# Optimization experiments

Measured on AMD Instinct MI355X. Metric: run time of the kernel, lower is better.

Reference implementation:

```python
import jax, jax.numpy as jnp
import numpy as np

N = 12288      # 12 * nside^2, nside=32
NBR = 20       # HEALpix graph neighbors
E = N * (NBR + 1)
B = 4
CIN = 8
COUT = 8
EPS = 1e-5


def _spmm(vals, row, col, x):
    """y = L @ x per batch/channel. x: [B, V, C]; L sparse COO (row, col, vals)."""
    b, v, c = x.shape
    x2 = x.transpose(1, 0, 2).reshape(v, b * c)          # [V, B*C]
    y = jax.ops.segment_sum(x2[col] * vals[:, None], row, num_segments=v)
    return y.reshape(v, b, c).transpose(1, 0, 2)          # [B, V, C]


def _cheb(vals, row, col, x, w, bias):
    """Chebyshev spectral graph conv: sum_k T_k(L) x W_k + b. w: [K, Fin, Fout]."""
    K = w.shape[0]
    xs = [x]
    if K > 1:
        xs.append(_spmm(vals, row, col, x))
    for _ in range(2, K):
        xs.append(2.0 * _spmm(vals, row, col, xs[-1]) - xs[-2])
    xk = jnp.stack(xs)                                    # [K, B, V, Fin]
    return jnp.einsum('kbvi,kio->bvo', xk, w) + bias


def _bn(x, g, b):
    # BatchNorm1d in training mode: stats over (batch, vertex) per channel
    m = x.mean(axis=(0, 1))
    v = x.var(axis=(0, 1))
    return (x - m) * jax.lax.rsqrt(v + EPS) * g + b


def setup_inputs() -> dict:
    key = jax.random.key(0)
    ks = jax.random.split(key, 12)
    x = jax.random.normal(ks[0], (B, N, CIN), jnp.float32)
    row = jnp.repeat(jnp.arange(N, dtype=jnp.int32), NBR + 1)
    nbr = jax.random.randint(ks[1], (N, NBR), 0, N, dtype=jnp.int32)
    col = jnp.concatenate([jnp.arange(N, dtype=jnp.int32)[:, None], nbr], axis=1).reshape(-1)
    edge_val = jax.random.normal(ks[2], (E,), jnp.float32) * 0.1

    def w(k, shape):
        return jax.random.normal(k, shape, jnp.float32) * 0.05

    return dict(
        x=x, edge_row=row, edge_col=col, edge_val=edge_val,
        conv1_w=w(ks[3], (3, CIN, 64)), conv1_b=jnp.zeros((64,), jnp.float32),
        bn1_g=jnp.ones((64,), jnp.float32), bn1_b=jnp.zeros((64,), jnp.float32),
        conv2_w=w(ks[4], (3, 64, 256)), conv2_b=jnp.zeros((256,), jnp.float32),
        bn2_g=jnp.ones((256,), jnp.float32), bn2_b=jnp.zeros((256,), jnp.float32),
        # 3 identical-shape bottlenecks stacked on leading axis
        bt_c1w=w(ks[5], (3, 1, 256, 64)), bt_c1b=jnp.zeros((3, 64), jnp.float32),
        bt_c2w=w(ks[6], (3, 3, 64, 64)), bt_c2b=jnp.zeros((3, 64), jnp.float32),
        bt_c3w=w(ks[7], (3, 1, 64, 256)), bt_c3b=jnp.zeros((3, 256), jnp.float32),
        bt_bn1g=jnp.ones((3, 64), jnp.float32), bt_bn1b=jnp.zeros((3, 64), jnp.float32),
        bt_bn2g=jnp.ones((3, 64), jnp.float32), bt_bn2b=jnp.zeros((3, 64), jnp.float32),
        bt_bn3g=jnp.ones((3, 256), jnp.float32), bt_bn3b=jnp.zeros((3, 256), jnp.float32),
        conv3_w=w(ks[8], (3, 256, COUT)), conv3_b=jnp.zeros((COUT,), jnp.float32),
    )


def reference(x, edge_row, edge_col, edge_val,
              conv1_w, conv1_b, bn1_g, bn1_b,
              conv2_w, conv2_b, bn2_g, bn2_b,
              bt_c1w, bt_c1b, bt_c2w, bt_c2b, bt_c3w, bt_c3b,
              bt_bn1g, bt_bn1b, bt_bn2g, bt_bn2b, bt_bn3g, bt_bn3b,
              conv3_w, conv3_b):
    L = (edge_val, edge_row, edge_col)

    def conv_block(h, w_, b_, g, bb):
        h = _cheb(*L, h, w_, b_)
        return jax.nn.relu(_bn(h, g, bb))

    def bottleneck(h, i):
        y = _cheb(*L, h, bt_c1w[i], bt_c1b[i])
        y = jax.nn.relu(_bn(y, bt_bn1g[i], bt_bn1b[i]))
        y = _cheb(*L, y, bt_c2w[i], bt_c2b[i])
        y = jax.nn.relu(_bn(y, bt_bn2g[i], bt_bn2b[i]))
        y = _cheb(*L, y, bt_c3w[i], bt_c3b[i])
        return _bn(y, bt_bn3g[i], bt_bn3b[i])

    h = conv_block(x, conv1_w, conv1_b, bn1_g, bn1_b)
    h = conv_block(h, conv2_w, conv2_b, bn2_g, bn2_b)
    for i in range(3):  # fixed, structurally distinct bottleneck blocks
        h = h + bottleneck(h, i)
    return _cheb(*L, h, conv3_w, conv3_b)  # [B, N, COUT]
```

## Files before the change

### kernel.cpp

```cpp
#include <hip/hip_runtime.h>

static constexpr int NBRS = 21;
static constexpr int Nv   = 12288;
static constexpr int BV   = 4 * Nv;
static constexpr int NE   = Nv * NBRS;
static constexpr float BN_EPS = 1e-5f;

typedef __bf16 bf16x4 __attribute__((ext_vector_type(4)));
typedef __bf16 bf16x8 __attribute__((ext_vector_type(8)));
typedef float  f32x4  __attribute__((ext_vector_type(4)));

__device__ __forceinline__ int xcd_swz(int bid, int grid)
{
    return (bid & 7) * (grid >> 3) + (bid >> 3);
}

template<int MODE>
__global__ __launch_bounds__(256)
void spmm8_kernel(float* __restrict__ y, const float* __restrict__ x,
                  const float* __restrict__ x0,
                  const int2* __restrict__ edges)
{
    int idx = xcd_swz(blockIdx.x, gridDim.x) * 256 + threadIdx.x;
    int c4 = idx & 1;
    int row = idx >> 1;
    int v = row % Nv;
    int b = row / Nv;
    int e0 = v * NBRS;
    const float4* x4 = (const float4*)x;
    float4 acc = {0.f, 0.f, 0.f, 0.f};
    #pragma unroll
    for (int j = 0; j < NBRS; ++j) {
        const int2 ed = edges[e0 + j];
        const float a = __int_as_float(ed.x);
        const int u = ed.y;
        float4 xv = x4[(size_t)(b * Nv + u) * 2 + c4];
        acc.x = fmaf(a, xv.x, acc.x);
        acc.y = fmaf(a, xv.y, acc.y);
        acc.z = fmaf(a, xv.z, acc.z);
        acc.w = fmaf(a, xv.w, acc.w);
    }
    if (MODE == 2) {
        float4 p = ((const float4*)x0)[idx];
        acc.x += p.x; acc.y += p.y; acc.z += p.z; acc.w += p.w;
    }
    ((float4*)y)[idx] = acc;
}

template<bool BNG>
__global__ __launch_bounds__(256)
void spmm64_kernel(__bf16* __restrict__ y, const __bf16* __restrict__ x,
                   const int2* __restrict__ edges,
                   const float* __restrict__ bn_a, const float* __restrict__ bn_b)
{
    int idx = xcd_swz(blockIdx.x, gridDim.x) * 256 + threadIdx.x;
    int q = idx % 8;
    int v = (idx / 8) % Nv;
    int b = idx / (8 * Nv);
    int e0 = v * NBRS;
    const bf16x8* x8 = (const bf16x8*)x;
    float4 aL, aH, bL, bH;
    if (BNG) {
        aL = ((const float4*)bn_a)[q * 2];     aH = ((const float4*)bn_a)[q * 2 + 1];
        bL = ((const float4*)bn_b)[q * 2];     bH = ((const float4*)bn_b)[q * 2 + 1];
    }
    float acc[8];
    #pragma unroll
    for (int t = 0; t < 8; ++t) acc[t] = 0.f;
    #pragma unroll
    for (int j = 0; j < NBRS; ++j) {
        const int2 ed = edges[e0 + j];
        const float a = __int_as_float(ed.x);
        const int u = ed.y;
        bf16x8 hv = x8[(size_t)(b * Nv + u) * 8 + q];
        float xv[8];
        #pragma unroll
        for (int t = 0; t < 8; ++t) xv[t] = (float)hv[t];
        if (BNG) {
            xv[0] = fmaxf(fmaf(xv[0], aL.x, bL.x), 0.f);
            xv[1] = fmaxf(fmaf(xv[1], aL.y, bL.y), 0.f);
            xv[2] = fmaxf(fmaf(xv[2], aL.z, bL.z), 0.f);
            xv[3] = fmaxf(fmaf(xv[3], aL.w, bL.w), 0.f);
            xv[4] = fmaxf(fmaf(xv[4], aH.x, bH.x), 0.f);
            xv[5] = fmaxf(fmaf(xv[5], aH.y, bH.y), 0.f);
            xv[6] = fmaxf(fmaf(xv[6], aH.z, bH.z), 0.f);
            xv[7] = fmaxf(fmaf(xv[7], aH.w, bH.w), 0.f);
        }
        #pragma unroll
        for (int t = 0; t < 8; ++t) acc[t] = fmaf(a, xv[t], acc[t]);
    }
    bf16x8 o;
    #pragma unroll
    for (int t = 0; t < 8; ++t) o[t] = (__bf16)acc[t];
    ((bf16x8*)y)[idx] = o;
}

__global__ __launch_bounds__(256)
void pack_all_kernel(const float* __restrict__ w1, const float* __restrict__ w2,
                     const float* __restrict__ c1, const float* __restrict__ c2,
                     const float* __restrict__ c3, const float* __restrict__ w3,
                     const float* __restrict__ b3,
                     const float* __restrict__ eval_, const int* __restrict__ col,
                     __bf16* __restrict__ wb, float* __restrict__ bpack,
                     int2* __restrict__ edges)
{
    int t = blockIdx.x * 256 + threadIdx.x;
    if (t >= 194560) {
        int i = t - 194560;
        if (i < 32) { bpack[i] = (i < 8) ? b3[i] : 0.f; return; }
        int e = t - 194592;
        if (e < NE) edges[e] = make_int2(__float_as_int(eval_[e]), col[e]);
        return;
    }
    const float* src; int KSRC, FOUT, FIN, local; bool fold = false, isW3 = false;
    if (t < 2048)        { src = w1;  KSRC = 24;  FOUT = 64;  FIN = 8;  local = t; fold = true; }
    else if (t < 51200)  { src = w2;  KSRC = 192; FOUT = 256; FIN = 64; local = t - 2048; fold = true; }
    else if (t < 100352) { int i = (t - 51200) / 16384;  src = c1 + (size_t)i * 16384;
                           KSRC = 256; FOUT = 64;  FIN = 256; local = (t - 51200) % 16384; }
    else if (t < 137216) { int i = (t - 100352) / 12288; src = c2 + (size_t)i * 12288;
                           KSRC = 192; FOUT = 64;  FIN = 64; local = (t - 100352) % 12288; fold = true; }
    else if (t < 186368) { int i = (t - 137216) / 16384; src = c3 + (size_t)i * 16384;
                           KSRC = 64;  FOUT = 256; FIN = 64; local = (t - 137216) % 16384; }
    else                 { src = w3;  KSRC = 256; FOUT = 32; FIN = 256; local = t - 186368; isW3 = true; }
    const int j    = local & 7;
    const int lane = (local >> 3) & 63;
    const int rest = local >> 9;
    const int NT = FOUT >> 4;
    const int nt = rest % NT;
    const int ks = rest / NT;
    const int k = ks * 32 + (lane >> 4) * 8 + j;
    const int o = nt * 16 + (lane & 15);
    float v = 0.f;
    if (isW3) {
        const int zj = o >> 3, oo = o & 7;
        if (zj == 0)      v = src[(size_t)k * 8 + oo] - src[(size_t)2 * 2048 + k * 8 + oo];
        else if (zj == 1) v = src[(size_t)2048 + k * 8 + oo];
        else if (zj == 2) v = 2.f * src[(size_t)2 * 2048 + k * 8 + oo];
    } else if (k < KSRC) {
        if (fold) {
            if (k < FIN)          v = src[(size_t)k * FOUT + o] - src[(size_t)(k + 2 * FIN) * FOUT + o];
            else if (k < 2 * FIN) v = src[(size_t)k * FOUT + o];
            else                  v = 2.f * src[(size_t)k * FOUT + o];
        } else {
            v = src[(size_t)k * FOUT + o];
        }
    }
    wb[t] = (__bf16)v;
}

template<int FOUT, int KFIN, int KPAD, int FIN, int NSRC,
         bool STATS, bool BN0, bool HAS_BIAS, bool PACKOUT, bool INBF, bool OUTBF,
         bool RESID = false, bool BASEBN = false, bool WRITEBACK = false>
__global__ __launch_bounds__(256)
void gemm_mfma_kernel(const void* __restrict__ x0, const void* __restrict__ x1,
                      const void* __restrict__ x2,
                      const __bf16* __restrict__ wp, const float* __restrict__ bias,
                      const float* __restrict__ bn_a, const float* __restrict__ bn_b,
                      const float* __restrict__ bn_a2, const float* __restrict__ bn_b2,
                      void* __restrict__ out, float2* __restrict__ partial,
                      __bf16* __restrict__ wbk)
{
    constexpr int NT    = FOUT / 16;
    constexpr int NSTEP = KPAD / 32;
    constexpr bool COLS = (NT % 4 == 0);
    constexpr int NT2   = COLS ? NT / 4 : NT;
    constexpr int LDKB  = KPAD + 8;
    constexpr int LDC   = FOUT + 4;
    constexpr size_t XS_B  = (size_t)64 * LDKB * 2;
    constexpr size_t RPK_B = COLS ? (size_t)16 * LDC * 4 : 0;
    constexpr size_t SMEM  = XS_B > RPK_B ? XS_B : RPK_B;
    __shared__ __align__(16) char smem[SMEM];
    __bf16* xs = (__bf16*)smem;

    const int tid = threadIdx.x;
    const int m0 = blockIdx.x * 64;

    constexpr int NF4 = 64 * (KPAD / 4);
    for (int f = tid; f < NF4; f += 256) {
        const int r  = f / (KPAD / 4);
        const int ki = (f % (KPAD / 4)) * 4;
        bf16x4 h;
        if (KFIN == KPAD || ki < KFIN) {
            int i; int kk;
            if constexpr (NSRC == 1) { i = ki; kk = 0; }
            else { kk = ki / FIN; i = ki % FIN; }
            if constexpr (RESID) {
                const __bf16* srcy = (const __bf16*)x0;
                const __bf16* srct = (const __bf16*)x1;
                bf16x4 hy = *(const bf16x4*)(srcy + (size_t)(m0 + r) * FIN + i);
                bf16x4 ht = *(const bf16x4*)(srct + (size_t)(m0 + r) * FIN + i);
                const float4 a4 = *(const float4*)(bn_a + i);
                const float4 b4 = *(const float4*)(bn_b + i);
                float bv0 = (float)ht[0], bv1 = (float)ht[1];
                float bv2 = (float)ht[2], bv3 = (float)ht[3];
                if constexpr (BASEBN) {
                    const float4 p4 = *(const float4*)(bn_a2 + i);
                    const float4 q4 = *(const float4*)(bn_b2 + i);
                    bv0 = fmaxf(fmaf(bv0, p4.x, q4.x), 0.f);
                    bv1 = fmaxf(fmaf(bv1, p4.y, q4.y), 0.f);
                    bv2 = fmaxf(fmaf(bv2, p4.z, q4.z), 0.f);
                    bv3 = fmaxf(fmaf(bv3, p4.w, q4.w), 0.f);
                }
                h[0] = (__bf16)(fmaf((float)hy[0], a4.x, b4.x) + bv0);
                h[1] = (__bf16)(fmaf((float)hy[1], a4.y, b4.y) + bv1);
                h[2] = (__bf16)(fmaf((float)hy[2], a4.z, b4.z) + bv2);
                h[3] = (__bf16)(fmaf((float)hy[3], a4.w, b4.w) + bv3);
                if constexpr (WRITEBACK)
                    *(bf16x4*)(wbk + (size_t)(m0 + r) * FIN + i) = h;
            } else if constexpr (INBF) {
                const __bf16* src = (kk == 0) ? (const __bf16*)x0
                                  : (kk == 1 ? (const __bf16*)x1 : (const __bf16*)x2);
                bf16x4 hv = *(const bf16x4*)(src + (size_t)(m0 + r) * FIN + i);
                if (BN0 && (NSRC == 1 || kk == 0)) {
                    const float4 a4 = *(const float4*)(bn_a + i);
                    const float4 b4 = *(const float4*)(bn_b + i);
                    h[0] = (__bf16)fmaxf(fmaf((float)hv[0], a4.x, b4.x), 0.f);
                    h[1] = (__bf16)fmaxf(fmaf((float)hv[1], a4.y, b4.y), 0.f);
                    h[2] = (__bf16)fmaxf(fmaf((float)hv[2], a4.z, b4.z), 0.f);
                    h[3] = (__bf16)fmaxf(fmaf((float)hv[3], a4.w, b4.w), 0.f);
                } else {
                    h = hv;
                }
            } else {
                const float* src = (kk == 0) ? (const float*)x0
                                 : (kk == 1 ? (const float*)x1 : (const float*)x2);
                float4 v = *(const float4*)(src + (size_t)(m0 + r) * FIN + i);
                if (BN0 && (NSRC == 1 || kk == 0)) {
                    const float4 a4 = *(const float4*)(bn_a + i);
                    const float4 b4 = *(const float4*)(bn_b + i);
                    v.x = fmaxf(fmaf(v.x, a4.x, b4.x), 0.f);
                    v.y = fmaxf(fmaf(v.y, a4.y, b4.y), 0.f);
                    v.z = fmaxf(fmaf(v.z, a4.z, b4.z), 0.f);
                    v.w = fmaxf(fmaf(v.w, a4.w, b4.w), 0.f);
                }
                h[0] = (__bf16)v.x; h[1] = (__bf16)v.y; h[2] = (__bf16)v.z; h[3] = (__bf16)v.w;
            }
        } else {
            h[0] = (__bf16)0.f; h[1] = (__bf16)0.f; h[2] = (__bf16)0.f; h[3] = (__bf16)0.f;
        }
        *(bf16x4*)(xs + (size_t)r * LDKB + ki) = h;
    }
    __syncthreads();

    const int lane = tid & 63;
    const int wv   = tid >> 6;
    const int lo   = lane & 15;
    const int hi   = lane >> 4;

    if constexpr (COLS) {
        f32x4 acc[4][NT2];
        #pragma unroll
        for (int mr = 0; mr < 4; ++mr)
            #pragma unroll
            for (int n = 0; n < NT2; ++n) acc[mr][n] = (f32x4){0.f, 0.f, 0.f, 0.f};

        #pragma unroll
        for (int ks = 0; ks < NSTEP; ++ks) {
            bf16x8 bfr[NT2];
            #pragma unroll
            for (int n = 0; n < NT2; ++n)
                bfr[n] = *(const bf16x8*)(wp + ((size_t)(ks * NT + wv * NT2 + n) * 64 + lane) * 8);
            bf16x8 afr[4];
            #pragma unroll
            for (int mr = 0; mr < 4; ++mr)
                afr[mr] = *(const bf16x8*)(xs + (size_t)(mr * 16 + lo) * LDKB + ks * 32 + hi * 8);
            #pragma unroll
            for (int n = 0; n < NT2; ++n)
                #pragma unroll
                for (int mr = 0; mr < 4; ++mr)
                    acc[mr][n] = __builtin_amdgcn_mfma_f32_16x16x32_bf16(afr[mr], bfr[n], acc[mr][n], 0, 0, 0);
        }

        #pragma unroll
        for (int n = 0; n < NT2; ++n) {
            const int o = wv * (FOUT / 4) + n * 16 + lo;
            const float bo = HAS_BIAS ? bias[o] : 0.f;
            #pragma unroll
            for (int mr = 0; mr < 4; ++mr)
                #pragma unroll
                for (int j = 0; j < 4; ++j) acc[mr][n][j] += bo;
        }

        if constexpr (STATS) {
            #pragma unroll
            for (int n = 0; n < NT2; ++n) {
                float s = 0.f, q = 0.f;
                #pragma unroll
                for (int mr = 0; mr < 4; ++mr)
                    #pragma unroll
                    for (int j = 0; j < 4; ++j) {
                        const float v = acc[mr][n][j];
                        s += v; q = fmaf(v, v, q);
                    }
                s += __shfl_xor(s, 16); q += __shfl_xor(q, 16);
                s += __shfl_xor(s, 32); q += __shfl_xor(q, 32);
                if (lane < 16) {
                    const int o = wv * (FOUT / 4) + n * 16 + lo;
                    partial[(size_t)o * gridDim.x + blockIdx.x] = make_float2(s, q);
                }
            }
        }

        float* cs = (float*)smem;
        #pragma unroll
        for (int mr = 0; mr < 4; ++mr) {
            __syncthreads();
            #pragma unroll
            for (int n = 0; n < NT2; ++n) {
                const int o = wv * (FOUT / 4) + n * 16 + lo;
                #pragma unroll
                for (int j = 0; j < 4; ++j)
                    cs[(size_t)(hi * 4 + j) * LDC + o] = acc[mr][n][j];
            }
            __syncthreads();
            for (int t = tid; t < 16 * (FOUT / 4); t += 256) {
                const int rr = t / (FOUT / 4);
                const int c4 = (t % (FOUT / 4)) * 4;
                const float4 v = *(const float4*)(cs + (size_t)rr * LDC + c4);
                if constexpr (OUTBF) {
                    bf16x4 hv;
                    hv[0] = (__bf16)v.x; hv[1] = (__bf16)v.y;
                    hv[2] = (__bf16)v.z; hv[3] = (__bf16)v.w;
                    *(bf16x4*)((__bf16*)out + (size_t)(m0 + mr * 16 + rr) * FOUT + c4) = hv;
                } else {
                    *(float4*)((float*)out + (size_t)(m0 + mr * 16 + rr) * FOUT + c4) = v;
                }
            }
        }
    } else {
        f32x4 acc[NT];
        #pragma unroll
        for (int nt = 0; nt < NT; ++nt) acc[nt] = (f32x4){0.f, 0.f, 0.f, 0.f};
        const int arow = wv * 16 + lo;
        #pragma unroll
        for (int ks = 0; ks < NSTEP; ++ks) {
            const bf16x8 a = *(const bf16x8*)(xs + (size_t)arow * LDKB + ks * 32 + hi * 8);
            #pragma unroll
            for (int nt = 0; nt < NT; ++nt) {
                const bf16x8 b = *(const bf16x8*)(wp + ((size_t)(ks * NT + nt) * 64 + lane) * 8);
                acc[nt] = __builtin_amdgcn_mfma_f32_16x16x32_bf16(a, b, acc[nt], 0, 0, 0);
            }
        }
        #pragma unroll
        for (int nt = 0; nt < NT; ++nt) {
            const int o = nt * 16 + lo;
            const float bo = HAS_BIAS ? bias[o] : 0.f;
            #pragma unroll
            for (int j = 0; j < 4; ++j) {
                const float v = acc[nt][j] + bo;
                const int m = m0 + wv * 16 + hi * 4 + j;
                if constexpr (PACKOUT) {
                    const int zj = o >> 3;
                    if (zj < 3) ((float*)out)[((size_t)zj * BV + m) * 8 + (o & 7)] = v;
                } else {
                    ((float*)out)[(size_t)m * FOUT + o] = v;
                }
            }
        }
    }
}

__global__ __launch_bounds__(256)
void bn_finalize_kernel(const float2* __restrict__ partial,
                        const float* __restrict__ g, const float* __restrict__ b,
                        float* __restrict__ a_out, float* __restrict__ b_out,
                        float invN, int nblk)
{
    __shared__ float2 red[4];
    const int c = blockIdx.x;
    const float2* p = partial + (size_t)c * nblk;
    float s = 0.f, ss = 0.f;
    for (int k = threadIdx.x; k < nblk; k += 256) {
        const float2 v = p[k];
        s += v.x; ss += v.y;
    }
    #pragma unroll
    for (int off = 32; off > 0; off >>= 1) {
        s  += __shfl_down(s, off);
        ss += __shfl_down(ss, off);
    }
    if ((threadIdx.x & 63) == 0) red[threadIdx.x >> 6] = make_float2(s, ss);
    __syncthreads();
    if (threadIdx.x == 0) {
        float ts = 0.f, tq = 0.f;
        #pragma unroll
        for (int i = 0; i < 4; ++i) { ts += red[i].x; tq += red[i].y; }
        const float m = ts * invN;
        const float var = tq * invN - m * m;
        const float a = g[c] * rsqrtf(var + BN_EPS);
        a_out[c] = a;
        b_out[c] = b[c] - m * a;
    }
}

extern "C" void kernel_launch(void* const* d_in, const int* in_sizes, int n_in,
                              void* d_out, int out_size, void* d_ws, size_t ws_size,
                              hipStream_t stream)
{
    const float* x       = (const float*)d_in[0];
    const int*   col     = (const int*)  d_in[2];
    const float* eval_   = (const float*)d_in[3];
    const float* conv1_w = (const float*)d_in[4];
    const float* conv1_b = (const float*)d_in[5];
    const float* bn1_g   = (const float*)d_in[6];
    const float* bn1_b   = (const float*)d_in[7];
    const float* conv2_w = (const float*)d_in[8];
    const float* conv2_b = (const float*)d_in[9];
    const float* bn2_g   = (const float*)d_in[10];
    const float* bn2_b   = (const float*)d_in[11];
    const float* bt_c1w  = (const float*)d_in[12];
    const float* bt_c1b  = (const float*)d_in[13];
    const float* bt_c2w  = (const float*)d_in[14];
    const float* bt_c2b  = (const float*)d_in[15];
    const float* bt_c3w  = (const float*)d_in[16];
    const float* bt_c3b  = (const float*)d_in[17];
    const float* btbn1g  = (const float*)d_in[18];
    const float* btbn1b  = (const float*)d_in[19];
    const float* btbn2g  = (const float*)d_in[20];
    const float* btbn2b  = (const float*)d_in[21];
    const float* btbn3g  = (const float*)d_in[22];
    const float* btbn3b  = (const float*)d_in[23];
    const float* conv3_w = (const float*)d_in[24];
    const float* conv3_b = (const float*)d_in[25];
    float* out = (float*)d_out;

    __bf16* h2b  = (__bf16*)d_ws;
    __bf16* y3b  = h2b + (size_t)BV * 256;
    __bf16* t64a = y3b + (size_t)BV * 256;
    __bf16* t64b = t64a + (size_t)BV * 64;
    __bf16* t64c = t64b + (size_t)BV * 64;
    __bf16* t64d = t64c + (size_t)BV * 64;
    float*  scr  = (float*)(t64d + (size_t)BV * 64);
    float*  aarr = scr + (size_t)BV * 32;
    float*  barr = aarr + 11 * 256;
    float*  bpack = barr + 11 * 256;
    __bf16* wb   = (__bf16*)(bpack + 32);
    __bf16* wp1  = wb;
    __bf16* wp2  = wp1 + 2048;
    __bf16* wpc1 = wp2 + 49152;
    __bf16* wpc2 = wpc1 + 49152;
    __bf16* wpc3 = wpc2 + 36864;
    __bf16* wp3  = wpc3 + 49152;
    float2* part = (float2*)(wp3 + 8192);
    int2*   edges = (int2*)(part + 256 * 768);

    float* t8a = scr;
    float* t8b = scr + (size_t)BV * 8;

    const float invN = 1.f / (float)BV;
    const int NGB  = BV / 64;
    const int NSP64 = BV * 8 / 256;
    const int NSP8  = BV * 2 / 256;

    pack_all_kernel<<<1769, 256, 0, stream>>>(conv1_w, conv2_w, bt_c1w, bt_c2w, bt_c3w,
                                              conv3_w, conv3_b, eval_, col, wb, bpack, edges);

    spmm8_kernel<0><<<NSP8, 256, 0, stream>>>(t8a, x, nullptr, edges);
    spmm8_kernel<0><<<NSP8, 256, 0, stream>>>(t8b, t8a, nullptr, edges);
    gemm_mfma_kernel<64, 24, 32, 8, 3, true, false, true, false, false, true>
        <<<NGB, 256, 0, stream>>>(x, t8a, t8b, wp1, conv1_b, nullptr, nullptr, nullptr, nullptr,
                                  t64c, part, nullptr);
    bn_finalize_kernel<<<64, 256, 0, stream>>>(part, bn1_g, bn1_b, aarr, barr, invN, NGB);

    spmm64_kernel<true ><<<NSP64, 256, 0, stream>>>(t64a, t64c, edges, aarr, barr);
    spmm64_kernel<false><<<NSP64, 256, 0, stream>>>(t64b, t64a, edges, nullptr, nullptr);
    gemm_mfma_kernel<256, 192, 192, 64, 3, true, true, true, false, true, true>
        <<<NGB, 256, 0, stream>>>(t64c, t64a, t64b, wp2, conv2_b, aarr, barr, nullptr, nullptr,
                                  h2b, part, nullptr);
    bn_finalize_kernel<<<256, 256, 0, stream>>>(part, bn2_g, bn2_b, aarr + 256, barr + 256, invN, NGB);

    for (int i = 0; i < 3; ++i) {
        float* aA = aarr + (2 + i * 3) * 256; float* bA = barr + (2 + i * 3) * 256;
        float* aB = aarr + (3 + i * 3) * 256; float* bB = barr + (3 + i * 3) * 256;
        float* aC = aarr + (4 + i * 3) * 256; float* bC = barr + (4 + i * 3) * 256;

        if (i == 0)
            gemm_mfma_kernel<64, 256, 256, 256, 1, true, true, true, false, true, true>
                <<<NGB, 256, 0, stream>>>(h2b, nullptr, nullptr, wpc1, bt_c1b,
                                          aarr + 256, barr + 256, nullptr, nullptr,
                                          t64c, part, nullptr);
        else if (i == 1)
            gemm_mfma_kernel<64, 256, 256, 256, 1, true, false, true, false, true, true, true, true, true>
                <<<NGB, 256, 0, stream>>>(y3b, h2b, nullptr, wpc1 + (size_t)1 * 16384, bt_c1b + 64,
                                          aarr + 4 * 256, barr + 4 * 256,
                                          aarr + 256, barr + 256,
                                          t64c, part, h2b);
        else
            gemm_mfma_kernel<64, 256, 256, 256, 1, true, false, true, false, true, true, true, false, true>
                <<<NGB, 256, 0, stream>>>(y3b, h2b, nullptr, wpc1 + (size_t)2 * 16384, bt_c1b + 128,
                                          aarr + 7 * 256, barr + 7 * 256,
                                          nullptr, nullptr,
                                          t64c, part, h2b);
        bn_finalize_kernel<<<64, 256, 0, stream>>>(part, btbn1g + i * 64, btbn1b + i * 64, aA, bA, invN, NGB);

        spmm64_kernel<true ><<<NSP64, 256, 0, stream>>>(t64a, t64c, edges, aA, bA);
        spmm64_kernel<false><<<NSP64, 256, 0, stream>>>(t64b, t64a, edges, nullptr, nullptr);
        gemm_mfma_kernel<64, 192, 192, 64, 3, true, true, true, false, true, true>
            <<<NGB, 256, 0, stream>>>(t64c, t64a, t64b, wpc2 + (size_t)i * 12288, bt_c2b + i * 64,
                                      aA, bA, nullptr, nullptr,
                                      t64d, part, nullptr);
        bn_finalize_kernel<<<64, 256, 0, stream>>>(part, btbn2g + i * 64, btbn2b + i * 64, aB, bB, invN, NGB);

        gemm_mfma_kernel<256, 64, 64, 64, 1, true, true, true, false, true, true>
            <<<NGB, 256, 0, stream>>>(t64d, nullptr, nullptr, wpc3 + (size_t)i * 16384, bt_c3b + i * 256,
                                      aB, bB, nullptr, nullptr,
                                      y3b, part, nullptr);
        bn_finalize_kernel<<<256, 256, 0, stream>>>(part, btbn3g + i * 256, btbn3b + i * 256, aC, bC, invN, NGB);
    }

    float* z0 = scr;
    float* z1 = z0 + (size_t)BV * 8;
    float* z2 = z1 + (size_t)BV * 8;
    float* ee = z2 + (size_t)BV * 8;
    float* aC2 = aarr + 10 * 256;
    float* bC2 = barr + 10 * 256;

    gemm_mfma_kernel<32, 256, 256, 256, 1, false, true, true, true, true, false, true>
        <<<NGB, 256, 0, stream>>>(y3b, h2b, nullptr, wp3, bpack,
                                  aC2, bC2, nullptr, nullptr,
                                  z0, nullptr, nullptr);

    spmm8_kernel<2><<<NSP8, 256, 0, stream>>>(ee, z2, z1, edges);
    spmm8_kernel<2><<<NSP8, 256, 0, stream>>>(out, ee, z0, edges);

    (void)in_sizes; (void)n_in; (void)out_size; (void)ws_size;
}
```

Before: 290.8 us.

## Replace BN finalize kernels with atomic stat accumulation and in-consumer finalize

GEMM kernels now atomically add per-channel sum and sum-of-squares into a global stats buffer instead of writing per-block partials. The separate bn_finalize launches are removed, and each consuming kernel (GEMM or spmm64) computes the scale and shift from the stats into shared memory at block start. This removes 11 kernel launches and their serial dependencies. In exchange it adds a memset, contention on the atomics, and redundant per-block finalize work, and the summation order becomes nondeterministic.

Result: slower. 392.6 us (+35.0%).

```diff
diff --git a/kernel.cpp b/kernel.cpp
--- a/kernel.cpp
+++ b/kernel.cpp
@@ -51,8 +51,21 @@
 __global__ __launch_bounds__(256)
 void spmm64_kernel(__bf16* __restrict__ y, const __bf16* __restrict__ x,
                    const int2* __restrict__ edges,
-                   const float* __restrict__ bn_a, const float* __restrict__ bn_b)
+                   const float* __restrict__ st, const float* __restrict__ g,
+                   const float* __restrict__ be, float invN)
 {
+    __shared__ __align__(16) float s_a[BNG ? 64 : 4];
+    __shared__ __align__(16) float s_b[BNG ? 64 : 4];
+    if (BNG) {
+        if (threadIdx.x < 64) {
+            const int c = threadIdx.x;
+            const float s = st[c], qq = st[256 + c];
+            const float m = s * invN;
+            const float a = g[c] * rsqrtf(qq * invN - m * m + BN_EPS);
+            s_a[c] = a; s_b[c] = be[c] - m * a;
+        }
+        __syncthreads();
+    }
     int idx = xcd_swz(blockIdx.x, gridDim.x) * 256 + threadIdx.x;
     int q = idx % 8;
     int v = (idx / 8) % Nv;
@@ -61,8 +74,8 @@
     const bf16x8* x8 = (const bf16x8*)x;
     float4 aL, aH, bL, bH;
     if (BNG) {
-        aL = ((const float4*)bn_a)[q * 2];     aH = ((const float4*)bn_a)[q * 2 + 1];
-        bL = ((const float4*)bn_b)[q * 2];     bH = ((const float4*)bn_b)[q * 2 + 1];
+        aL = *(const float4*)(s_a + q * 8);     aH = *(const float4*)(s_a + q * 8 + 4);
+        bL = *(const float4*)(s_b + q * 8);     bH = *(const float4*)(s_b + q * 8 + 4);
     }
     float acc[8];
     #pragma unroll
@@ -155,10 +168,12 @@
 void gemm_mfma_kernel(const void* __restrict__ x0, const void* __restrict__ x1,
                       const void* __restrict__ x2,
                       const __bf16* __restrict__ wp, const float* __restrict__ bias,
-                      const float* __restrict__ bn_a, const float* __restrict__ bn_b,
-                      const float* __restrict__ bn_a2, const float* __restrict__ bn_b2,
-                      void* __restrict__ out, float2* __restrict__ partial,
-                      __bf16* __restrict__ wbk)
+                      const float* __restrict__ st1, const float* __restrict__ g1,
+                      const float* __restrict__ be1,
+                      const float* __restrict__ st2, const float* __restrict__ g2,
+                      const float* __restrict__ be2,
+                      void* __restrict__ out, float* __restrict__ stats_out,
+                      __bf16* __restrict__ wbk, float invN)
 {
     constexpr int NT    = FOUT / 16;
     constexpr int NSTEP = KPAD / 32;
@@ -166,14 +181,36 @@
     constexpr int NT2   = COLS ? NT / 4 : NT;
     constexpr int LDKB  = KPAD + 8;
     constexpr int LDC   = FOUT + 4;
+    constexpr bool ANYBN = BN0 || RESID || BASEBN;
     constexpr size_t XS_B  = (size_t)64 * LDKB * 2;
     constexpr size_t RPK_B = COLS ? (size_t)16 * LDC * 4 : 0;
     constexpr size_t SMEM  = XS_B > RPK_B ? XS_B : RPK_B;
     __shared__ __align__(16) char smem[SMEM];
+    __shared__ __align__(16) float abst[ANYBN ? 1024 : 4];
     __bf16* xs = (__bf16*)smem;
+    float* ab1a = abst;        float* ab1b = abst + 256;
+    float* ab2a = abst + 512;  float* ab2b = abst + 768;
 
     const int tid = threadIdx.x;
     const int m0 = blockIdx.x * 64;
+
+    if constexpr (BN0 || RESID) {
+        for (int c = tid; c < FIN; c += 256) {
+            const float s = st1[c], qq = st1[256 + c];
+            const float m = s * invN;
+            const float a = g1[c] * rsqrtf(qq * invN - m * m + BN_EPS);
+            ab1a[c] = a; ab1b[c] = be1[c] - m * a;
+        }
+    }
+    if constexpr (BASEBN) {
+        for (int c = tid; c < FIN; c += 256) {
+            const float s = st2[c], qq = st2[256 + c];
+            const float m = s * invN;
+            const float a = g2[c] * rsqrtf(qq * invN - m * m + BN_EPS);
+            ab2a[c] = a; ab2b[c] = be2[c] - m * a;
+        }
+    }
+    if constexpr (ANYBN) __syncthreads();
 
     constexpr int NF4 = 64 * (KPAD / 4);
     for (int f = tid; f < NF4; f += 256) {
@@ -189,13 +226,13 @@
                 const __bf16* srct = (const __bf16*)x1;
                 bf16x4 hy = *(const bf16x4*)(srcy + (size_t)(m0 + r) * FIN + i);
                 bf16x4 ht = *(const bf16x4*)(srct + (size_t)(m0 + r) * FIN + i);
-                const float4 a4 = *(const float4*)(bn_a + i);
-                const float4 b4 = *(const float4*)(bn_b + i);
+                const float4 a4 = *(const float4*)(ab1a + i);
+                const float4 b4 = *(const float4*)(ab1b + i);
                 float bv0 = (float)ht[0], bv1 = (float)ht[1];
                 float bv2 = (float)ht[2], bv3 = (float)ht[3];
                 if constexpr (BASEBN) {
-                    const float4 p4 = *(const float4*)(bn_a2 + i);
-                    const float4 q4 = *(const float4*)(bn_b2 + i);
+                    const float4 p4 = *(const float4*)(ab2a + i);
+                    const float4 q4 = *(const float4*)(ab2b + i);
                     bv0 = fmaxf(fmaf(bv0, p4.x, q4.x), 0.f);
                     bv1 = fmaxf(fmaf(bv1, p4.y, q4.y), 0.f);
                     bv2 = fmaxf(fmaf(bv2, p4.z, q4.z), 0.f);
@@ -212,8 +249,8 @@
                                   : (kk == 1 ? (const __bf16*)x1 : (const __bf16*)x2);
                 bf16x4 hv = *(const bf16x4*)(src + (size_t)(m0 + r) * FIN + i);
                 if (BN0 && (NSRC == 1 || kk == 0)) {
-                    const float4 a4 = *(const float4*)(bn_a + i);
-                    const float4 b4 = *(const float4*)(bn_b + i);
+                    const float4 a4 = *(const float4*)(ab1a + i);
+                    const float4 b4 = *(const float4*)(ab1b + i);
                     h[0] = (__bf16)fmaxf(fmaf((float)hv[0], a4.x, b4.x), 0.f);
                     h[1] = (__bf16)fmaxf(fmaf((float)hv[1], a4.y, b4.y), 0.f);
                     h[2] = (__bf16)fmaxf(fmaf((float)hv[2], a4.z, b4.z), 0.f);
@@ -226,8 +263,8 @@
                                  : (kk == 1 ? (const float*)x1 : (const float*)x2);
                 float4 v = *(const float4*)(src + (size_t)(m0 + r) * FIN + i);
                 if (BN0 && (NSRC == 1 || kk == 0)) {
-                    const float4 a4 = *(const float4*)(bn_a + i);
-                    const float4 b4 = *(const float4*)(bn_b + i);
+                    const float4 a4 = *(const float4*)(ab1a + i);
+                    const float4 b4 = *(const float4*)(ab1b + i);
                     v.x = fmaxf(fmaf(v.x, a4.x, b4.x), 0.f);
                     v.y = fmaxf(fmaf(v.y, a4.y, b4.y), 0.f);
                     v.z = fmaxf(fmaf(v.z, a4.z, b4.z), 0.f);
@@ -296,7 +333,8 @@
                 s += __shfl_xor(s, 32); q += __shfl_xor(q, 32);
                 if (lane < 16) {
                     const int o = wv * (FOUT / 4) + n * 16 + lo;
-                    partial[(size_t)o * gridDim.x + blockIdx.x] = make_float2(s, q);
+                    atomicAdd(&stats_out[o], s);
+                    atomicAdd(&stats_out[256 + o], q);
                 }
             }
         }
@@ -357,39 +395,6 @@
                 }
             }
         }
-    }
-}
-
-__global__ __launch_bounds__(256)
-void bn_finalize_kernel(const float2* __restrict__ partial,
-                        const float* __restrict__ g, const float* __restrict__ b,
-                        float* __restrict__ a_out, float* __restrict__ b_out,
-                        float invN, int nblk)
-{
-    __shared__ float2 red[4];
-    const int c = blockIdx.x;
-    const float2* p = partial + (size_t)c * nblk;
-    float s = 0.f, ss = 0.f;
-    for (int k = threadIdx.x; k < nblk; k += 256) {
-        const float2 v = p[k];
-        s += v.x; ss += v.y;
-    }
-    #pragma unroll
-    for (int off = 32; off > 0; off >>= 1) {
-        s  += __shfl_down(s, off);
-        ss += __shfl_down(ss, off);
-    }
-    if ((threadIdx.x & 63) == 0) red[threadIdx.x >> 6] = make_float2(s, ss);
-    __syncthreads();
-    if (threadIdx.x == 0) {
-        float ts = 0.f, tq = 0.f;
-        #pragma unroll
-        for (int i = 0; i < 4; ++i) { ts += red[i].x; tq += red[i].y; }
-        const float m = ts * invN;
-        const float var = tq * invN - m * m;
-        const float a = g[c] * rsqrtf(var + BN_EPS);
-        a_out[c] = a;
-        b_out[c] = b[c] - m * a;
     }
 }
 
@@ -431,9 +436,7 @@
     __bf16* t64c = t64b + (size_t)BV * 64;
     __bf16* t64d = t64c + (size_t)BV * 64;
     float*  scr  = (float*)(t64d + (size_t)BV * 64);
-    float*  aarr = scr + (size_t)BV * 32;
-    float*  barr = aarr + 11 * 256;
-    float*  bpack = barr + 11 * 256;
+    float*  bpack = scr + (size_t)BV * 32;
     __bf16* wb   = (__bf16*)(bpack + 32);
     __bf16* wp1  = wb;
     __bf16* wp2  = wp1 + 2048;
@@ -441,8 +444,8 @@
     __bf16* wpc2 = wpc1 + 49152;
     __bf16* wpc3 = wpc2 + 36864;
     __bf16* wp3  = wpc3 + 49152;
-    float2* part = (float2*)(wp3 + 8192);
-    int2*   edges = (int2*)(part + 256 * 768);
+    float*  stats = (float*)(wp3 + 8192);
+    int2*   edges = (int2*)(stats + 11 * 512);
 
     float* t8a = scr;
     float* t8b = scr + (size_t)BV * 8;
@@ -452,73 +455,74 @@
     const int NSP64 = BV * 8 / 256;
     const int NSP8  = BV * 2 / 256;
 
+    float* ST0 = stats;
+    float* ST1 = stats + 512;
+
+    hipMemsetAsync(stats, 0, 11 * 512 * sizeof(float), stream);
+
     pack_all_kernel<<<1769, 256, 0, stream>>>(conv1_w, conv2_w, bt_c1w, bt_c2w, bt_c3w,
                                               conv3_w, conv3_b, eval_, col, wb, bpack, edges);
 
     spmm8_kernel<0><<<NSP8, 256, 0, stream>>>(t8a, x, nullptr, edges);
     spmm8_kernel<0><<<NSP8, 256, 0, stream>>>(t8b, t8a, nullptr, edges);
     gemm_mfma_kernel<64, 24, 32, 8, 3, true, false, true, false, false, true>
-        <<<NGB, 256, 0, stream>>>(x, t8a, t8b, wp1, conv1_b, nullptr, nullptr, nullptr, nullptr,
-                                  t64c, part, nullptr);
-    bn_finalize_kernel<<<64, 256, 0, stream>>>(part, bn1_g, bn1_b, aarr, barr, invN, NGB);
-
-    spmm64_kernel<true ><<<NSP64, 256, 0, stream>>>(t64a, t64c, edges, aarr, barr);
-    spmm64_kernel<false><<<NSP64, 256, 0, stream>>>(t64b, t64a, edges, nullptr, nullptr);
+        <<<NGB, 256, 0, stream>>>(x, t8a, t8b, wp1, conv1_b,
+                                  nullptr, nullptr, nullptr, nullptr, nullptr, nullptr,
+                                  t64c, ST0, nullptr, invN);
+
+    spmm64_kernel<true ><<<NSP64, 256, 0, stream>>>(t64a, t64c, edges, ST0, bn1_g, bn1_b, invN);
+    spmm64_kernel<false><<<NSP64, 256, 0, stream>>>(t64b, t64a, edges, nullptr, nullptr, nullptr, invN);
     gemm_mfma_kernel<256, 192, 192, 64, 3, true, true, true, false, true, true>
-        <<<NGB, 256, 0, stream>>>(t64c, t64a, t64b, wp2, conv2_b, aarr, barr, nullptr, nullptr,
-                                  h2b, part, nullptr);
-    bn_finalize_kernel<<<256, 256, 0, stream>>>(part, bn2_g, bn2_b, aarr + 256, barr + 256, invN, NGB);
+        <<<NGB, 256, 0, stream>>>(t64c, t64a, t64b, wp2, conv2_b,
+                                  ST0, bn1_g, bn1_b, nullptr, nullptr, nullptr,
+                                  h2b, ST1, nullptr, invN);
 
     for (int i = 0; i < 3; ++i) {
-        float* aA = aarr + (2 + i * 3) * 256; float* bA = barr + (2 + i * 3) * 256;
-        float* aB = aarr + (3 + i * 3) * 256; float* bB = barr + (3 + i * 3) * 256;
-        float* aC = aarr + (4 + i * 3) * 256; float* bC = barr + (4 + i * 3) * 256;
+        float* STA = stats + (2 + i * 3) * 512;
+        float* STB = stats + (3 + i * 3) * 512;
+        float* STC = stats + (4 + i * 3) * 512;
 
         if (i == 0)
             gemm_mfma_kernel<64, 256, 256, 256, 1, true, true, true, false, true, true>
                 <<<NGB, 256, 0, stream>>>(h2b, nullptr, nullptr, wpc1, bt_c1b,
-                                          aarr + 256, barr + 256, nullptr, nullptr,
-                                          t64c, part, nullptr);
+                                          ST1, bn2_g, bn2_b, nullptr, nullptr, nullptr,
+                                          t64c, STA, nullptr, invN);
         else if (i == 1)
             gemm_mfma_kernel<64, 256, 256, 256, 1, true, false, true, false, true, true, true, true, true>
                 <<<NGB, 256, 0, stream>>>(y3b, h2b, nullptr, wpc1 + (size_t)1 * 16384, bt_c1b + 64,
-                                          aarr + 4 * 256, barr + 4 * 256,
-                                          aarr + 256, barr + 256,
-                                          t64c, part, h2b);
+                                          stats + 4 * 512, btbn3g, btbn3b,
+                                          ST1, bn2_g, bn2_b,
+                                          t64c, STA, h2b, invN);
         else
             gemm_mfma_kernel<64, 256, 256, 256, 1, true, false, true, false, true, true, true, false, true>
                 <<<NGB, 256, 0, stream>>>(y3b, h2b, nullptr, wpc1 + (size_t)2 * 16384, bt_c1b + 128,
-                                          aarr + 7 * 256, barr + 7 * 256,
-                                          nullptr, nullptr,
-                                          t64c, part, h2b);
-        bn_finalize_kernel<<<64, 256, 0, stream>>>(part, btbn1g + i * 64, btbn1b + i * 64, aA, bA, invN, NGB);
-
-        spmm64_kernel<true ><<<NSP64, 256, 0, stream>>>(t64a, t64c, edges, aA, bA);
-        spmm64_kernel<false><<<NSP64, 256, 0, stream>>>(t64b, t64a, edges, nullptr, nullptr);
+                                          stats + 7 * 512, btbn3g + 256, btbn3b + 256,
+                                          nullptr, nullptr, nullptr,
+                                          t64c, STA, h2b, invN);
+
+        spmm64_kernel<true ><<<NSP64, 256, 0, stream>>>(t64a, t64c, edges, STA, btbn1g + i * 64, btbn1b + i * 64, invN);
+        spmm64_kernel<false><<<NSP64, 256, 0, stream>>>(t64b, t64a, edges, nullptr, nullptr, nullptr, invN);
         gemm_mfma_kernel<64, 192, 192, 64, 3, true, true, true, false, true, true>
             <<<NGB, 256, 0, stream>>>(t64c, t64a, t64b, wpc2 + (size_t)i * 12288, bt_c2b + i * 64,
-                                      aA, bA, nullptr, nullptr,
-                                      t64d, part, nullptr);
-        bn_finalize_kernel<<<64, 256, 0, stream>>>(part, btbn2g + i * 64, btbn2b + i * 64, aB, bB, invN, NGB);
+                                      STA, btbn1g + i * 64, btbn1b + i * 64, nullptr, nullptr, nullptr,
+                                      t64d, STB, nullptr, invN);
 
         gemm_mfma_kernel<256, 64, 64, 64, 1, true, true, true, false, true, true>
             <<<NGB, 256, 0, stream>>>(t64d, nullptr, nullptr, wpc3 + (size_t)i * 16384, bt_c3b + i * 256,
-                                      aB, bB, nullptr, nullptr,
-                                      y3b, part, nullptr);
-        bn_finalize_kernel<<<256, 256, 0, stream>>>(part, btbn3g + i * 256, btbn3b + i * 256, aC, bC, invN, NGB);
+                                      STB, btbn2g + i * 64, btbn2b + i * 64, nullptr, nullptr, nullptr,
+                                      y3b, STC, nullptr, invN);
     }
 
     float* z0 = scr;
     float* z1 = z0 + (size_t)BV * 8;
     float* z2 = z1 + (size_t)BV * 8;
     float* ee = z2 + (size_t)BV * 8;
-    float* aC2 = aarr + 10 * 256;
-    float* bC2 = barr + 10 * 256;
 
     gemm_mfma_kernel<32, 256, 256, 256, 1, false, true, true, true, true, false, true>
         <<<NGB, 256, 0, stream>>>(y3b, h2b, nullptr, wp3, bpack,
-                                  aC2, bC2, nullptr, nullptr,
-                                  z0, nullptr, nullptr);
+                                  stats + 10 * 512, btbn3g + 512, btbn3b + 512,
+                                  nullptr, nullptr, nullptr,
+                                  z0, nullptr, nullptr, invN);
 
     spmm8_kernel<2><<<NSP8, 256, 0, stream>>>(ee, z2, z1, edges);
     spmm8_kernel<2><<<NSP8, 256, 0, stream>>>(out, ee, z0, edges);
```
